# Optimization experiments

Hardware: AMD Instinct MI355X
Metric: run time of the kernel (lower is better)

## Reference

```python
import jax, jax.numpy as jnp
import numpy as np

EPS = 1e-6


def setup_inputs() -> dict:
    key = jax.random.key(0)
    ks = jax.random.split(key, 5)
    B, NH, S, DQK, DV = 2, 8, 1024, 256, 512
    return {
        "q": jax.random.normal(ks[0], (B, NH, S, DQK), dtype=jnp.float32),
        "k": jax.random.normal(ks[1], (B, NH, S, DQK), dtype=jnp.float32),
        "v": jax.random.normal(ks[2], (B, NH, S, DV), dtype=jnp.float32),
        "i_preact": jax.random.normal(ks[3], (B, NH, S), dtype=jnp.float32),
        "f_preact": jax.random.normal(ks[4], (B, NH, S), dtype=jnp.float32),
    }


def reference(q, k, v, i_preact, f_preact):
    B, NH, S, DQK = q.shape
    DV = v.shape[-1]
    inv_sqrt_d = jnp.asarray(1.0 / np.sqrt(DQK), dtype=q.dtype)
    eps = jnp.asarray(EPS, dtype=q.dtype)

    C0 = jnp.zeros((B, NH, DQK, DV), dtype=q.dtype)
    n0 = jnp.zeros((B, NH, DQK), dtype=q.dtype)
    m0 = jnp.zeros((B, NH), dtype=q.dtype)

    def step(carry, xs):
        C, n, m = carry
        q_t, k_t, v_t, i_t, f_t = xs  # [B,NH,DQK],[B,NH,DQK],[B,NH,DV],[B,NH],[B,NH]
        # f_log = -log(1 + exp(-f)) = log_sigmoid(f)
        f_log = jax.nn.log_sigmoid(f_t)
        m_new = jnp.maximum(f_log + m, i_t)
        f_gate = jnp.exp(f_log + m - m_new)
        i_gate = jnp.exp(i_t - m_new)
        kv_outer = k_t[..., :, None] * v_t[..., None, :]  # [B,NH,DQK,DV]
        C = f_gate[..., None, None] * C + i_gate[..., None, None] * kv_outer
        n = f_gate[..., None] * n + i_gate[..., None] * k_t
        q_scaled = q_t * inv_sqrt_d
        h_num = jnp.einsum("bhdv,bhd->bhv", C, q_scaled)
        qn_dot = jnp.sum(n * q_scaled, axis=-1, keepdims=True)  # [B,NH,1]
        h_den = jnp.maximum(jnp.abs(qn_dot), jnp.exp(-m_new)[..., None]) + eps
        h_t = h_num / h_den
        return (C, n, m_new), h_t

    # time-major scan over S
    xs = (
        jnp.moveaxis(q, 2, 0),
        jnp.moveaxis(k, 2, 0),
        jnp.moveaxis(v, 2, 0),
        jnp.moveaxis(i_preact, 2, 0),
        jnp.moveaxis(f_preact, 2, 0),
    )
    (C, n, m), h_tm = jax.lax.scan(step, (C0, n0, m0), xs)
    h = jnp.moveaxis(h_tm, 0, 2)  # [B,NH,S,DV]
    return h, C, n, m
```

## Files before the change

### kernel.cpp

```cpp
#include <hip/hip_runtime.h>
#include <math.h>

#define SEQ   1024
#define DQ    256
#define DVD   512
#define NHH   16
#define EPSF  1e-6f
#define INV_SQRT_D 0.0625f

typedef __attribute__((ext_vector_type(8)))  short short8v;
typedef __attribute__((ext_vector_type(16))) float f32x16;

#define WS_FG    0
#define WS_IG    (NHH*SEQ)
#define WS_ELIM  (2*NHH*SEQ)
#define WS_HDEN  (3*NHH*SEQ)
#define WS_AT    (4*NHH*SEQ)
#define WS_CS    (5*NHH*SEQ)
#define WS_AC    (6*NHH*SEQ)
#define WS_BVEC  (WS_AC + NHH*16)
#define WS_SMALL_FLOATS (WS_BVEC + NHH*16*DQ)

#define QBF_OFF  ((size_t)WS_SMALL_FLOATS * 4)
#define KBF_OFF  (QBF_OFF + (size_t)NHH*SEQ*DQ*2)
#define VTB_OFF  (KBF_OFF + (size_t)NHH*SEQ*DQ*2)
#define KUT_OFF  (VTB_OFF + (size_t)NHH*DVD*SEQ*2)

__device__ __forceinline__ unsigned short f2bf(float f) {
  unsigned int u = __float_as_uint(f);
  return (unsigned short)((u + 0x7fffu + ((u >> 16) & 1u)) >> 16);
}

__device__ __forceinline__ void gl_lds16(const void* g, void* l) {
  __builtin_amdgcn_global_load_lds(
      (const __attribute__((address_space(1))) unsigned int*)g,
      (__attribute__((address_space(3))) unsigned int*)l, 16, 0, 0);
}

__global__ __launch_bounds__(256) void prep_kernel(
    const float* __restrict__ kin, const float* __restrict__ vin,
    const float* __restrict__ ipre, const float* __restrict__ fpre,
    float* __restrict__ ws,
    unsigned short* __restrict__ k_bf, unsigned short* __restrict__ vt_bf,
    unsigned short* __restrict__ kut, float* __restrict__ m_out) {
  __shared__ float lk[64][257];
  __shared__ float swsum[4], swmax[4];
  __shared__ float bndF[16], bndM[16], fin2[2];
  __shared__ float cfg[64], cig[64], cut[64];

  const int b = blockIdx.x;
  if (b < 256) {
    const int hh = b >> 4, c = b & 15;
    const int d = threadIdx.x;
    const int lane = d & 63, wid = d >> 6;
    const int tbase = hh*SEQ + c*64;
    const size_t base = (size_t)tbase * DQ;

    #pragma unroll 4
    for (int tt = 0; tt < 64; ++tt) {
      const float val = kin[base + (size_t)tt*DQ + d];
      lk[tt][d] = val;
      k_bf[base + (size_t)tt*DQ + d] = f2bf(val);
    }

    const float4 f4 = *(const float4*)(fpre + hh*SEQ + 4*d);
    const float4 i4 = *(const float4*)(ipre + hh*SEQ + 4*d);
    float fv[4] = {f4.x, f4.y, f4.z, f4.w};
    float iv[4] = {i4.x, i4.y, i4.z, i4.w};
    float fl[4], F[4];
    float s = 0.f;
    #pragma unroll
    for (int j = 0; j < 4; ++j) {
      fl[j] = fminf(fv[j], 0.f) - log1pf(expf(-fabsf(fv[j])));
      s += fl[j]; F[j] = s;
    }
    float wsc = s;
    #pragma unroll
    for (int off = 1; off < 64; off <<= 1) {
      float o = __shfl_up(wsc, off, 64);
      if (lane >= off) wsc += o;
    }
    if (lane == 63) swsum[wid] = wsc;
    __syncthreads();
    float woff = 0.f;
    #pragma unroll
    for (int i = 0; i < 4; ++i) { float t = swsum[i]; if (i < wid) woff += t; }
    const float Fexc = woff + (wsc - s);
    #pragma unroll
    for (int j = 0; j < 4; ++j) F[j] += Fexc;

    float zser[4];
    float zs = -INFINITY;
    #pragma unroll
    for (int j = 0; j < 4; ++j) {
      zs = fmaxf(zs, iv[j] - F[j]); zser[j] = zs;
    }
    float zmI = zs;
    #pragma unroll
    for (int off = 1; off < 64; off <<= 1) {
      float o = __shfl_up(zmI, off, 64);
      if (lane >= off) zmI = fmaxf(zmI, o);
    }
    if (lane == 63) swmax[wid] = zmI;
    float zexcl = __shfl_up(zmI, 1, 64);
    if (lane == 0) zexcl = -INFINITY;
    __syncthreads();
    float zoffW = -INFINITY;
    #pragma unroll
    for (int i = 0; i < 4; ++i) { float t = swmax[i]; if (i < wid) zoffW = fmaxf(zoffW, t); }
    const float zPexc = fmaxf(zoffW, zexcl);

    float mprev = Fexc + fmaxf(zPexc, 0.f);
    float m_[4], fg_[4], ig_[4];
    #pragma unroll
    for (int j = 0; j < 4; ++j) {
      const float zP = fmaxf(zPexc, zser[j]);
      m_[j] = F[j] + fmaxf(zP, 0.f);
      fg_[j] = expf(fl[j] + mprev - m_[j]);
      ig_[j] = expf(iv[j] - m_[j]);
      mprev = m_[j];
    }

    if ((d & 15) == 15) { bndF[d >> 4] = F[3]; bndM[d >> 4] = m_[3]; }
    if (d == 255)       { fin2[0] = F[3]; fin2[1] = m_[3]; }
    const int q0 = d - 16*c;
    if (q0 >= 0 && q0 < 16) {
      #pragma unroll
      for (int j = 0; j < 4; ++j) { cfg[q0*4 + j] = fg_[j]; cig[q0*4 + j] = ig_[j]; }
    }
    if (c == 0) {
      float4 o;
      o.x=fg_[0]; o.y=fg_[1]; o.z=fg_[2]; o.w=fg_[3];
      *(float4*)(ws + WS_FG + hh*SEQ + 4*d) = o;
      o.x=ig_[0]; o.y=ig_[1]; o.z=ig_[2]; o.w=ig_[3];
      *(float4*)(ws + WS_IG + hh*SEQ + 4*d) = o;
      o.x=expf(-m_[0]); o.y=expf(-m_[1]); o.z=expf(-m_[2]); o.w=expf(-m_[3]);
      *(float4*)(ws + WS_ELIM + hh*SEQ + 4*d) = o;
      o.x=F[0]-m_[0]; o.y=F[1]-m_[1]; o.z=F[2]-m_[2]; o.w=F[3]-m_[3];
      *(float4*)(ws + WS_AT + hh*SEQ + 4*d) = o;
      o.x=iv[0]-F[0]; o.y=iv[1]-F[1]; o.z=iv[2]-F[2]; o.w=iv[3]-F[3];
      *(float4*)(ws + WS_CS + hh*SEQ + 4*d) = o;
      if (d == 255) m_out[hh] = m_[3];
    }
    __syncthreads();
    if (c == 0 && d < 16) {
      const float Fp = d ? bndF[d-1] : 0.f;
      const float mp = d ? bndM[d-1] : 0.f;
      ws[WS_AC + hh*16 + d] = expf((bndF[d] - Fp) + (mp - bndM[d]));
    }
    if (q0 >= 0 && q0 < 16) {
      const float Fe = fin2[0], me = fin2[1];
      #pragma unroll
      for (int j = 0; j < 4; ++j)
        cut[q0*4 + j] = expf(Fe - F[j] + iv[j] - me);
    }
    __syncthreads();

    float nb = 0.f;
    #pragma unroll 8
    for (int tt = 0; tt < 64; ++tt) nb = cfg[tt]*nb + cig[tt]*lk[tt][d];
    ws[WS_BVEC + (hh*16 + c)*DQ + d] = nb;
    #pragma unroll
    for (int g = 0; g < 8; ++g) {
      short8v pk;
      #pragma unroll
      for (int j = 0; j < 8; ++j) {
        const int tt = g*8 + j;
        pk[j] = (short)f2bf(cut[tt] * lk[tt][d]);
      }
      *(short8v*)(kut + ((size_t)(hh*DQ + d))*SEQ + c*64 + g*8) = pk;
    }
  } else {
    const int b2 = b - 256;
    const int hh = b2 >> 5, tg = b2 & 31;
    const int tx = threadIdx.x & 31, ty = threadIdx.x >> 5;
    float (*tile)[33] = (float(*)[33])lk;
    for (int vt = 0; vt < 16; ++vt) {
      #pragma unroll
      for (int i = 0; i < 4; ++i)
        tile[ty + 8*i][tx] =
            vin[((size_t)(hh*SEQ + tg*32 + ty + 8*i))*DVD + vt*32 + tx];
      __syncthreads();
      #pragma unroll
      for (int i = 0; i < 4; ++i)
        vt_bf[((size_t)(hh*DVD + vt*32 + ty + 8*i))*SEQ + tg*32 + tx] =
            f2bf(tile[tx][ty + 8*i]);
      __syncthreads();
    }
  }
}

__global__ __launch_bounds__(256) void hden_kernel(
    const float* __restrict__ kin, const float* __restrict__ qin,
    float* __restrict__ ws, unsigned short* __restrict__ q_bf,
    float* __restrict__ n_out) {
  const int hh = blockIdx.x >> 4;
  const int c  = blockIdx.x & 15;
  const int d  = threadIdx.x;
  __shared__ float pbuf[64][DQ];
  __shared__ float spart[64][4];

  float n = 0.f;
  for (int j = 0; j < c; ++j)
    n = ws[WS_AC + hh*16 + j]*n + ws[WS_BVEC + (hh*16 + j)*DQ + d];
  if (c == 15) {
    const float nf = ws[WS_AC + hh*16 + 15]*n +
                     ws[WS_BVEC + (hh*16 + 15)*DQ + d];
    n_out[hh*DQ + d] = nf;
  }

  const int tbase = hh*SEQ + c*64;
  const size_t base = (size_t)tbase * DQ;
  #pragma unroll 4
  for (int tt = 0; tt < 64; ++tt) {
    const float fg = ws[WS_FG + tbase + tt];
    const float ig = ws[WS_IG + tbase + tt];
    n = fg*n + ig*kin[base + (size_t)tt*DQ + d];
    const float qv = qin[base + (size_t)tt*DQ + d];
    q_bf[base + (size_t)tt*DQ + d] = f2bf(qv * INV_SQRT_D);
    pbuf[tt][d] = n * qv;
  }
  __syncthreads();

  {
    const int tt = d >> 2, qd = d & 3;
    float s = 0.f;
    #pragma unroll 8
    for (int j = 0; j < 64; ++j)
      s += pbuf[tt][qd*64 + ((j + d) & 63)];
    spart[tt][qd] = s;
  }
  __syncthreads();
  if (d < 64) {
    const float tot = (spart[d][0] + spart[d][1]) + (spart[d][2] + spart[d][3]);
    const float qn = tot * INV_SQRT_D;
    const float hd = fmaxf(fabsf(qn), ws[WS_ELIM + tbase + d]) + EPSF;
    ws[WS_HDEN + tbase + d] = hd;
  }
}

__global__ __launch_bounds__(512, 2) void attn_kernel(
    const unsigned short* __restrict__ q_bf,
    const unsigned short* __restrict__ k_bf,
    const unsigned short* __restrict__ vt_bf,
    const float* __restrict__ ws,
    float* __restrict__ h_out) {
  const int idx = blockIdx.x;
  const int hh = idx & 15;
  const int pr = (idx >> 4) & 7;
  const int vh = idx >> 7;

  const int tid = threadIdx.x;
  const int w = tid >> 6, lane = tid & 63, l31 = lane & 31, hl = lane >> 5;
  const int tsub = w >> 2;
  const int sblk = w & 3;
  const int vsub = w & 3;

  __shared__ unsigned short Klds[128*256];
  __shared__ unsigned short Vtlds[256*128];
  __shared__ unsigned short Plds[64*128];
  __shared__ float c_lds[128];

  const float* a_g  = ws + WS_AT;
  const float* c_g  = ws + WS_CS;
  const float* hd_g = ws + WS_HDEN;

  auto stage = [&](int c) {
    const int s0 = c*128;
    #pragma unroll
    for (int p = 0; p < 8; ++p) {
      int u = p*512 + tid;
      int row = u >> 5, slot = u & 31;
      const unsigned short* src = k_bf +
          ((size_t)(hh*SEQ + s0 + row))*DQ + ((slot ^ (row & 31))*8);
      gl_lds16(src, (char*)Klds + (p*8 + w)*1024);
    }
    #pragma unroll
    for (int p = 0; p < 8; ++p) {
      int u = p*512 + tid;
      int row = u >> 4, slot = u & 15;
      const unsigned short* src = vt_bf +
          ((size_t)(hh*DVD + vh*256 + row))*SEQ + s0 + ((slot ^ (row & 15))*8);
      gl_lds16(src, (char*)Vtlds + (p*8 + w)*1024);
    }
    if (tid < 128) c_lds[tid] = c_g[hh*SEQ + s0 + tid];
  };

  for (int tile = 0; tile < 2; ++tile) {
    const int qi  = tile ? pr : (15 - pr);
    const int nch = (qi >> 1) + 1;

    const int tq = qi*64 + tsub*32 + l31;
    const float a_t = a_g[hh*SEQ + tq];
    short8v qfrag[16];
    #pragma unroll
    for (int d = 0; d < 16; ++d)
      qfrag[d] = *(const short8v*)(q_bf + ((size_t)(hh*SEQ + tq))*DQ + d*16 + hl*8);

    f32x16 acc0 = {}, acc1 = {};

    stage(0);
    __syncthreads();

    for (int c = 0; c < nch; ++c) {
      const int s0 = c*128;
      f32x16 sacc = {};
      const int srow = sblk*32 + l31;
      #pragma unroll
      for (int d = 0; d < 16; ++d) {
        short8v af = *(const short8v*)&Klds[srow*256 + (((d*2 + hl) ^ (srow & 31))*8)];
        sacc = __builtin_amdgcn_mfma_f32_32x32x16_bf16(af, qfrag[d], sacc, 0, 0, 0);
      }
      const int prow = tsub*32 + l31;
      #pragma unroll
      for (int i = 0; i < 8; ++i) {
        const int r0 = 2*i;
        const int sl = sblk*32 + (r0 & 3) + 8*(r0 >> 2) + 4*hl;
        const int sg = s0 + sl;
        const float c0 = c_lds[sl];
        const float c1 = c_lds[sl + 1];
        const float p0 = (sg     <= tq) ? __expf(a_t + c0) * sacc[r0]     : 0.f;
        const float p1 = (sg + 1 <= tq) ? __expf(a_t + c1) * sacc[r0 + 1] : 0.f;
        unsigned int pk;
        asm volatile("v_cvt_pk_bf16_f32 %0, %1, %2" : "=v"(pk) : "v"(p0), "v"(p1));
        const int byte = sl*2;
        const int slot = byte >> 4, rem = byte & 15;
        *(unsigned int*)((char*)Plds + prow*256 + ((slot ^ (prow & 15))<<4) + rem) = pk;
      }
      __syncthreads();

      #pragma unroll
      for (int ss = 0; ss < 8; ++ss) {
        const int arow = tsub*32 + l31;
        short8v pa = *(const short8v*)&Plds[arow*128 + (((ss*2 + hl) ^ (arow & 15))*8)];
        const int vr0 = vsub*64 + l31;
        const int slotB = (ss*2 + hl) ^ (l31 & 15);
        short8v vb0 = *(const short8v*)&Vtlds[vr0*128 + slotB*8];
        short8v vb1 = *(const short8v*)&Vtlds[(vr0 + 32)*128 + slotB*8];
        acc0 = __builtin_amdgcn_mfma_f32_32x32x16_bf16(pa, vb0, acc0, 0, 0, 0);
        acc1 = __builtin_amdgcn_mfma_f32_32x32x16_bf16(pa, vb1, acc1, 0, 0, 0);
      }
      __syncthreads();
      if (c + 1 < nch) { stage(c + 1); __syncthreads(); }
    }

    #pragma unroll
    for (int r = 0; r < 16; ++r) {
      const int tl = tsub*32 + (r & 3) + 8*(r >> 2) + 4*hl;
      const int tg = qi*64 + tl;
      const float inv = 1.0f / hd_g[hh*SEQ + tg];
      const size_t ob = ((size_t)(hh*SEQ + tg))*DVD + vh*256 + vsub*64 + l31;
      h_out[ob]      = acc0[r] * inv;
      h_out[ob + 32] = acc1[r] * inv;
    }
  }
}

__global__ __launch_bounds__(256, 2) void cgemm_kernel(
    const unsigned short* __restrict__ kut,
    const unsigned short* __restrict__ vt,
    float* __restrict__ C_out) {
  const int b = blockIdx.x;
  const int hh = b >> 4;
  const int mt = (b >> 3) & 1;
  const int nt = b & 7;
  const int tid = threadIdx.x;
  const int w = tid >> 6, lane = tid & 63, l31 = lane & 31, hl = lane >> 5;
  const int mr = w >> 1;
  const int nc = w & 1;

  __shared__ unsigned short Alds[128*64];
  __shared__ unsigned short Blds[64*64];

  f32x16 acc0 = {}, acc1 = {};
  for (int c = 0; c < 16; ++c) {
    const int t0 = c*64;
    #pragma unroll
    for (int p = 0; p < 4; ++p) {
      int u = p*256 + tid; int row = u >> 3, slot = u & 7;
      const unsigned short* src = kut +
          ((size_t)(hh*DQ + mt*128 + row))*SEQ + t0 + ((slot ^ (row & 7))*8);
      gl_lds16(src, (char*)Alds + (p*4 + w)*1024);
    }
    #pragma unroll
    for (int p = 0; p < 2; ++p) {
      int u = p*256 + tid; int row = u >> 3, slot = u & 7;
      const unsigned short* src = vt +
          ((size_t)(hh*DVD + nt*64 + row))*SEQ + t0 + ((slot ^ (row & 7))*8);
      gl_lds16(src, (char*)Blds + (p*4 + w)*1024);
    }
    __syncthreads();
    #pragma unroll
    for (int ks = 0; ks < 4; ++ks) {
      const int br = nc*32 + l31;
      short8v bf_ = *(const short8v*)&Blds[br*64 + (((ks*2 + hl) ^ (br & 7))*8)];
      const int ar0 = mr*64 + l31, ar1 = ar0 + 32;
      short8v a0 = *(const short8v*)&Alds[ar0*64 + (((ks*2 + hl) ^ (ar0 & 7))*8)];
      short8v a1 = *(const short8v*)&Alds[ar1*64 + (((ks*2 + hl) ^ (ar1 & 7))*8)];
      acc0 = __builtin_amdgcn_mfma_f32_32x32x16_bf16(a0, bf_, acc0, 0, 0, 0);
      acc1 = __builtin_amdgcn_mfma_f32_32x32x16_bf16(a1, bf_, acc1, 0, 0, 0);
    }
    __syncthreads();
  }
  #pragma unroll
  for (int r = 0; r < 16; ++r) {
    const int dl = (r & 3) + 8*(r >> 2) + 4*hl;
    const int d0 = mt*128 + mr*64 + dl;
    const size_t ob = ((size_t)(hh*DQ + d0))*DVD + nt*64 + nc*32 + l31;
    C_out[ob]            = acc0[r];
    C_out[ob + 32*DVD]   = acc1[r];
  }
}

extern "C" void kernel_launch(void* const* d_in, const int* in_sizes, int n_in,
                              void* d_out, int out_size, void* d_ws, size_t ws_size,
                              hipStream_t stream) {
  const float* q  = (const float*)d_in[0];
  const float* k  = (const float*)d_in[1];
  const float* v  = (const float*)d_in[2];
  const float* ip = (const float*)d_in[3];
  const float* fp = (const float*)d_in[4];

  float* h_out = (float*)d_out;
  float* C_out = h_out + (size_t)NHH*SEQ*DVD;
  float* n_out = C_out + (size_t)NHH*DQ*DVD;
  float* m_out = n_out + NHH*DQ;
  float* ws    = (float*)d_ws;

  unsigned short* q_bf  = (unsigned short*)((char*)d_ws + QBF_OFF);
  unsigned short* k_bf  = (unsigned short*)((char*)d_ws + KBF_OFF);
  unsigned short* vt_bf = (unsigned short*)((char*)d_ws + VTB_OFF);
  unsigned short* kut   = (unsigned short*)((char*)d_ws + KUT_OFF);

  prep_kernel<<<768, 256, 0, stream>>>(k, v, ip, fp, ws, k_bf, vt_bf, kut, m_out);
  hden_kernel<<<NHH*16, 256, 0, stream>>>(k, q, ws, q_bf, n_out);
  attn_kernel<<<256, 512, 0, stream>>>(q_bf, k_bf, vt_bf, ws, h_out);
  cgemm_kernel<<<256, 256, 0, stream>>>(kut, vt_bf, C_out);
}
```

Baseline: 99.73 us.

## Split attention work into one query tile per block and stream V from global

```diff
diff --git a/kernel.cpp b/kernel.cpp
--- a/kernel.cpp
+++ b/kernel.cpp
@@ -239,16 +239,20 @@
   }
 }
 
-__global__ __launch_bounds__(512, 2) void attn_kernel(
+__global__ __launch_bounds__(512, 4) void attn_kernel(
     const unsigned short* __restrict__ q_bf,
     const unsigned short* __restrict__ k_bf,
     const unsigned short* __restrict__ vt_bf,
     const float* __restrict__ ws,
     float* __restrict__ h_out) {
-  const int idx = blockIdx.x;
+  const int b = blockIdx.x;
+  const int phase = b >> 8;
+  const int idx = b & 255;
   const int hh = idx & 15;
-  const int pr = (idx >> 4) & 7;
-  const int vh = idx >> 7;
+  const int vh = (idx >> 4) & 1;
+  const int qq = idx >> 5;
+  const int qi = phase ? (15 - qq) : qq;
+  const int nch = (qi >> 1) + 1;
 
   const int tid = threadIdx.x;
   const int w = tid >> 6, lane = tid & 63, l31 = lane & 31, hl = lane >> 5;
@@ -257,15 +261,23 @@
   const int vsub = w & 3;
 
   __shared__ unsigned short Klds[128*256];
-  __shared__ unsigned short Vtlds[256*128];
   __shared__ unsigned short Plds[64*128];
-  __shared__ float c_lds[128];
 
   const float* a_g  = ws + WS_AT;
-  const float* c_g  = ws + WS_CS;
+  const float* c_g  = ws + WS_CS + hh*SEQ;
   const float* hd_g = ws + WS_HDEN;
 
-  auto stage = [&](int c) {
+  const int tq = qi*64 + tsub*32 + l31;
+  const float a_t = a_g[hh*SEQ + tq];
+  const unsigned short* qp = q_bf + ((size_t)(hh*SEQ + tq))*DQ + hl*8;
+
+  const int vr0 = vsub*64 + l31;
+  const unsigned short* vp0 = vt_bf + ((size_t)(hh*DVD + vh*256 + vr0))*SEQ + hl*8;
+  const unsigned short* vp1 = vp0 + (size_t)32*SEQ;
+
+  f32x16 acc0 = {}, acc1 = {};
+
+  auto stageK = [&](int c) {
     const int s0 = c*128;
     #pragma unroll
     for (int p = 0; p < 8; ++p) {
@@ -275,84 +287,65 @@
           ((size_t)(hh*SEQ + s0 + row))*DQ + ((slot ^ (row & 31))*8);
       gl_lds16(src, (char*)Klds + (p*8 + w)*1024);
     }
-    #pragma unroll
-    for (int p = 0; p < 8; ++p) {
-      int u = p*512 + tid;
-      int row = u >> 4, slot = u & 15;
-      const unsigned short* src = vt_bf +
-          ((size_t)(hh*DVD + vh*256 + row))*SEQ + s0 + ((slot ^ (row & 15))*8);
-      gl_lds16(src, (char*)Vtlds + (p*8 + w)*1024);
-    }
-    if (tid < 128) c_lds[tid] = c_g[hh*SEQ + s0 + tid];
   };
 
-  for (int tile = 0; tile < 2; ++tile) {
-    const int qi  = tile ? pr : (15 - pr);
-    const int nch = (qi >> 1) + 1;
-
-    const int tq = qi*64 + tsub*32 + l31;
-    const float a_t = a_g[hh*SEQ + tq];
-    short8v qfrag[16];
-    #pragma unroll
-    for (int d = 0; d < 16; ++d)
-      qfrag[d] = *(const short8v*)(q_bf + ((size_t)(hh*SEQ + tq))*DQ + d*16 + hl*8);
-
-    f32x16 acc0 = {}, acc1 = {};
-
-    stage(0);
-    __syncthreads();
-
-    for (int c = 0; c < nch; ++c) {
-      const int s0 = c*128;
-      f32x16 sacc = {};
-      const int srow = sblk*32 + l31;
-      #pragma unroll
-      for (int d = 0; d < 16; ++d) {
-        short8v af = *(const short8v*)&Klds[srow*256 + (((d*2 + hl) ^ (srow & 31))*8)];
-        sacc = __builtin_amdgcn_mfma_f32_32x32x16_bf16(af, qfrag[d], sacc, 0, 0, 0);
-      }
-      const int prow = tsub*32 + l31;
-      #pragma unroll
-      for (int i = 0; i < 8; ++i) {
-        const int r0 = 2*i;
-        const int sl = sblk*32 + (r0 & 3) + 8*(r0 >> 2) + 4*hl;
-        const int sg = s0 + sl;
-        const float c0 = c_lds[sl];
-        const float c1 = c_lds[sl + 1];
-        const float p0 = (sg     <= tq) ? __expf(a_t + c0) * sacc[r0]     : 0.f;
-        const float p1 = (sg + 1 <= tq) ? __expf(a_t + c1) * sacc[r0 + 1] : 0.f;
-        unsigned int pk;
-        asm volatile("v_cvt_pk_bf16_f32 %0, %1, %2" : "=v"(pk) : "v"(p0), "v"(p1));
-        const int byte = sl*2;
-        const int slot = byte >> 4, rem = byte & 15;
-        *(unsigned int*)((char*)Plds + prow*256 + ((slot ^ (prow & 15))<<4) + rem) = pk;
-      }
-      __syncthreads();
-
-      #pragma unroll
-      for (int ss = 0; ss < 8; ++ss) {
-        const int arow = tsub*32 + l31;
-        short8v pa = *(const short8v*)&Plds[arow*128 + (((ss*2 + hl) ^ (arow & 15))*8)];
-        const int vr0 = vsub*64 + l31;
-        const int slotB = (ss*2 + hl) ^ (l31 & 15);
-        short8v vb0 = *(const short8v*)&Vtlds[vr0*128 + slotB*8];
-        short8v vb1 = *(const short8v*)&Vtlds[(vr0 + 32)*128 + slotB*8];
-        acc0 = __builtin_amdgcn_mfma_f32_32x32x16_bf16(pa, vb0, acc0, 0, 0, 0);
-        acc1 = __builtin_amdgcn_mfma_f32_32x32x16_bf16(pa, vb1, acc1, 0, 0, 0);
-      }
-      __syncthreads();
-      if (c + 1 < nch) { stage(c + 1); __syncthreads(); }
-    }
-
-    #pragma unroll
-    for (int r = 0; r < 16; ++r) {
-      const int tl = tsub*32 + (r & 3) + 8*(r >> 2) + 4*hl;
-      const int tg = qi*64 + tl;
-      const float inv = 1.0f / hd_g[hh*SEQ + tg];
-      const size_t ob = ((size_t)(hh*SEQ + tg))*DVD + vh*256 + vsub*64 + l31;
-      h_out[ob]      = acc0[r] * inv;
-      h_out[ob + 32] = acc1[r] * inv;
-    }
+  stageK(0);
+  __syncthreads();
+
+  for (int c = 0; c < nch; ++c) {
+    const int s0 = c*128;
+    f32x16 sacc = {};
+    const int srow = sblk*32 + l31;
+    #pragma unroll
+    for (int d = 0; d < 16; ++d) {
+      short8v qf = *(const short8v*)(qp + d*16);
+      short8v af = *(const short8v*)&Klds[srow*256 + (((d*2 + hl) ^ (srow & 31))*8)];
+      sacc = __builtin_amdgcn_mfma_f32_32x32x16_bf16(af, qf, sacc, 0, 0, 0);
+    }
+    const int prow = tsub*32 + l31;
+    #pragma unroll
+    for (int i = 0; i < 8; ++i) {
+      const int r0 = 2*i;
+      const int sl = sblk*32 + (r0 & 3) + 8*(r0 >> 2) + 4*hl;
+      const int sg = s0 + sl;
+      const float c0 = c_g[sg];
+      const float c1 = c_g[sg + 1];
+      const float p0 = (sg     <= tq) ? __expf(a_t + c0) * sacc[r0]     : 0.f;
+      const float p1 = (sg + 1 <= tq) ? __expf(a_t + c1) * sacc[r0 + 1] : 0.f;
+      unsigned int pk;
+      asm volatile("v_cvt_pk_bf16_f32 %0, %1, %2" : "=v"(pk) : "v"(p0), "v"(p1));
+      const int byte = sl*2;
+      const int slot = byte >> 4, rem = byte & 15;
+      *(unsigned int*)((char*)Plds + prow*256 + ((slot ^ (prow & 15))<<4) + rem) = pk;
+    }
+    __syncthreads();
+
+    short8v vf0[8], vf1[8];
+    #pragma unroll
+    for (int ss = 0; ss < 8; ++ss) {
+      vf0[ss] = *(const short8v*)(vp0 + s0 + ss*16);
+      vf1[ss] = *(const short8v*)(vp1 + s0 + ss*16);
+    }
+    if (c + 1 < nch) stageK(c + 1);
+
+    #pragma unroll
+    for (int ss = 0; ss < 8; ++ss) {
+      const int arow = tsub*32 + l31;
+      short8v pa = *(const short8v*)&Plds[arow*128 + (((ss*2 + hl) ^ (arow & 15))*8)];
+      acc0 = __builtin_amdgcn_mfma_f32_32x32x16_bf16(pa, vf0[ss], acc0, 0, 0, 0);
+      acc1 = __builtin_amdgcn_mfma_f32_32x32x16_bf16(pa, vf1[ss], acc1, 0, 0, 0);
+    }
+    __syncthreads();
+  }
+
+  #pragma unroll
+  for (int r = 0; r < 16; ++r) {
+    const int tl = tsub*32 + (r & 3) + 8*(r >> 2) + 4*hl;
+    const int tg = qi*64 + tl;
+    const float inv = 1.0f / hd_g[hh*SEQ + tg];
+    const size_t ob = ((size_t)(hh*SEQ + tg))*DVD + vh*256 + vsub*64 + l31;
+    h_out[ob]      = acc0[r] * inv;
+    h_out[ob + 32] = acc1[r] * inv;
   }
 }
 
@@ -434,6 +427,6 @@
 
   prep_kernel<<<768, 256, 0, stream>>>(k, v, ip, fp, ws, k_bf, vt_bf, kut, m_out);
   hden_kernel<<<NHH*16, 256, 0, stream>>>(k, q, ws, q_bf, n_out);
-  attn_kernel<<<256, 512, 0, stream>>>(q_bf, k_bf, vt_bf, ws, h_out);
+  attn_kernel<<<512, 512, 0, stream>>>(q_bf, k_bf, vt_bf, ws, h_out);
   cgemm_kernel<<<256, 256, 0, stream>>>(kut, vt_bf, C_out);
 }
```

Measured after the change: 208.4 us. 109% more time.

## Merge hden and C-gemm into one launch and split attention tiles per block

Applied to the files above, without the earlier changes.

```diff
diff --git a/kernel.cpp b/kernel.cpp
--- a/kernel.cpp
+++ b/kernel.cpp
@@ -190,52 +190,110 @@
   }
 }
 
-__global__ __launch_bounds__(256) void hden_kernel(
+__global__ __launch_bounds__(256) void aux_kernel(
     const float* __restrict__ kin, const float* __restrict__ qin,
     float* __restrict__ ws, unsigned short* __restrict__ q_bf,
-    float* __restrict__ n_out) {
-  const int hh = blockIdx.x >> 4;
-  const int c  = blockIdx.x & 15;
-  const int d  = threadIdx.x;
-  __shared__ float pbuf[64][DQ];
-  __shared__ float spart[64][4];
-
-  float n = 0.f;
-  for (int j = 0; j < c; ++j)
-    n = ws[WS_AC + hh*16 + j]*n + ws[WS_BVEC + (hh*16 + j)*DQ + d];
-  if (c == 15) {
-    const float nf = ws[WS_AC + hh*16 + 15]*n +
-                     ws[WS_BVEC + (hh*16 + 15)*DQ + d];
-    n_out[hh*DQ + d] = nf;
-  }
-
-  const int tbase = hh*SEQ + c*64;
-  const size_t base = (size_t)tbase * DQ;
-  #pragma unroll 4
-  for (int tt = 0; tt < 64; ++tt) {
-    const float fg = ws[WS_FG + tbase + tt];
-    const float ig = ws[WS_IG + tbase + tt];
-    n = fg*n + ig*kin[base + (size_t)tt*DQ + d];
-    const float qv = qin[base + (size_t)tt*DQ + d];
-    q_bf[base + (size_t)tt*DQ + d] = f2bf(qv * INV_SQRT_D);
-    pbuf[tt][d] = n * qv;
-  }
-  __syncthreads();
-
-  {
-    const int tt = d >> 2, qd = d & 3;
-    float s = 0.f;
-    #pragma unroll 8
-    for (int j = 0; j < 64; ++j)
-      s += pbuf[tt][qd*64 + ((j + d) & 63)];
-    spart[tt][qd] = s;
-  }
-  __syncthreads();
-  if (d < 64) {
-    const float tot = (spart[d][0] + spart[d][1]) + (spart[d][2] + spart[d][3]);
-    const float qn = tot * INV_SQRT_D;
-    const float hd = fmaxf(fabsf(qn), ws[WS_ELIM + tbase + d]) + EPSF;
-    ws[WS_HDEN + tbase + d] = hd;
+    float* __restrict__ n_out,
+    const unsigned short* __restrict__ kut,
+    const unsigned short* __restrict__ vt,
+    float* __restrict__ C_out) {
+  __shared__ __align__(16) char smem[66560];
+  const int b = blockIdx.x;
+
+  if (b < 256) {
+    float (*pbuf)[DQ] = (float(*)[DQ])smem;
+    float (*spart)[4] = (float(*)[4])(smem + 65536);
+    const int hh = b >> 4;
+    const int c  = b & 15;
+    const int d  = threadIdx.x;
+
+    float n = 0.f;
+    for (int j = 0; j < c; ++j)
+      n = ws[WS_AC + hh*16 + j]*n + ws[WS_BVEC + (hh*16 + j)*DQ + d];
+    if (c == 15) {
+      const float nf = ws[WS_AC + hh*16 + 15]*n +
+                       ws[WS_BVEC + (hh*16 + 15)*DQ + d];
+      n_out[hh*DQ + d] = nf;
+    }
+
+    const int tbase = hh*SEQ + c*64;
+    const size_t base = (size_t)tbase * DQ;
+    #pragma unroll 4
+    for (int tt = 0; tt < 64; ++tt) {
+      const float fg = ws[WS_FG + tbase + tt];
+      const float ig = ws[WS_IG + tbase + tt];
+      n = fg*n + ig*kin[base + (size_t)tt*DQ + d];
+      const float qv = qin[base + (size_t)tt*DQ + d];
+      q_bf[base + (size_t)tt*DQ + d] = f2bf(qv * INV_SQRT_D);
+      pbuf[tt][d] = n * qv;
+    }
+    __syncthreads();
+
+    {
+      const int tt = d >> 2, qd = d & 3;
+      float s = 0.f;
+      #pragma unroll 8
+      for (int j = 0; j < 64; ++j)
+        s += pbuf[tt][qd*64 + ((j + d) & 63)];
+      spart[tt][qd] = s;
+    }
+    __syncthreads();
+    if (d < 64) {
+      const float tot = (spart[d][0] + spart[d][1]) + (spart[d][2] + spart[d][3]);
+      const float qn = tot * INV_SQRT_D;
+      const float hd = fmaxf(fabsf(qn), ws[WS_ELIM + tbase + d]) + EPSF;
+      ws[WS_HDEN + tbase + d] = hd;
+    }
+  } else {
+    unsigned short* Alds = (unsigned short*)smem;
+    unsigned short* Blds = (unsigned short*)(smem + 16384);
+    const int b2 = b - 256;
+    const int hh = b2 >> 4;
+    const int mt = (b2 >> 3) & 1;
+    const int nt = b2 & 7;
+    const int tid = threadIdx.x;
+    const int w = tid >> 6, lane = tid & 63, l31 = lane & 31, hl = lane >> 5;
+    const int mr = w >> 1;
+    const int nc = w & 1;
+
+    f32x16 acc0 = {}, acc1 = {};
+    for (int c = 0; c < 16; ++c) {
+      const int t0 = c*64;
+      #pragma unroll
+      for (int p = 0; p < 4; ++p) {
+        int u = p*256 + tid; int row = u >> 3, slot = u & 7;
+        const unsigned short* src = kut +
+            ((size_t)(hh*DQ + mt*128 + row))*SEQ + t0 + ((slot ^ (row & 7))*8);
+        gl_lds16(src, (char*)Alds + (p*4 + w)*1024);
+      }
+      #pragma unroll
+      for (int p = 0; p < 2; ++p) {
+        int u = p*256 + tid; int row = u >> 3, slot = u & 7;
+        const unsigned short* src = vt +
+            ((size_t)(hh*DVD + nt*64 + row))*SEQ + t0 + ((slot ^ (row & 7))*8);
+        gl_lds16(src, (char*)Blds + (p*4 + w)*1024);
+      }
+      __syncthreads();
+      #pragma unroll
+      for (int ks = 0; ks < 4; ++ks) {
+        const int br = nc*32 + l31;
+        short8v bf_ = *(const short8v*)&Blds[br*64 + (((ks*2 + hl) ^ (br & 7))*8)];
+        const int ar0 = mr*64 + l31, ar1 = ar0 + 32;
+        short8v a0 = *(const short8v*)&Alds[ar0*64 + (((ks*2 + hl) ^ (ar0 & 7))*8)];
+        short8v a1 = *(const short8v*)&Alds[ar1*64 + (((ks*2 + hl) ^ (ar1 & 7))*8)];
+        acc0 = __builtin_amdgcn_mfma_f32_32x32x16_bf16(a0, bf_, acc0, 0, 0, 0);
+        acc1 = __builtin_amdgcn_mfma_f32_32x32x16_bf16(a1, bf_, acc1, 0, 0, 0);
+      }
+      __syncthreads();
+    }
+    #pragma unroll
+    for (int r = 0; r < 16; ++r) {
+      const int dl = (r & 3) + 8*(r >> 2) + 4*hl;
+      const int d0 = mt*128 + mr*64 + dl;
+      const size_t ob = ((size_t)(hh*DQ + d0))*DVD + nt*64 + nc*32 + l31;
+      C_out[ob]            = acc0[r];
+      C_out[ob + 32*DVD]   = acc1[r];
+    }
   }
 }
 
@@ -245,10 +303,14 @@
     const unsigned short* __restrict__ vt_bf,
     const float* __restrict__ ws,
     float* __restrict__ h_out) {
-  const int idx = blockIdx.x;
+  const int b = blockIdx.x;
+  const int phase = b >> 8;
+  const int idx = b & 255;
   const int hh = idx & 15;
-  const int pr = (idx >> 4) & 7;
-  const int vh = idx >> 7;
+  const int vh = (idx >> 4) & 1;
+  const int qq = idx >> 5;
+  const int qi = phase ? (15 - qq) : qq;
+  const int nch = (qi >> 1) + 1;
 
   const int tid = threadIdx.x;
   const int w = tid >> 6, lane = tid & 63, l31 = lane & 31, hl = lane >> 5;
@@ -264,6 +326,16 @@
   const float* a_g  = ws + WS_AT;
   const float* c_g  = ws + WS_CS;
   const float* hd_g = ws + WS_HDEN;
+
+  const int tq = qi*64 + tsub*32 + l31;
+  const float a_t = a_g[hh*SEQ + tq];
+
+  short8v qfrag[16];
+  #pragma unroll
+  for (int d = 0; d < 16; ++d)
+    qfrag[d] = *(const short8v*)(q_bf + ((size_t)(hh*SEQ + tq))*DQ + d*16 + hl*8);
+
+  f32x16 acc0 = {}, acc1 = {};
 
   auto stage = [&](int c) {
     const int s0 = c*128;
@@ -286,129 +358,59 @@
     if (tid < 128) c_lds[tid] = c_g[hh*SEQ + s0 + tid];
   };
 
-  for (int tile = 0; tile < 2; ++tile) {
-    const int qi  = tile ? pr : (15 - pr);
-    const int nch = (qi >> 1) + 1;
-
-    const int tq = qi*64 + tsub*32 + l31;
-    const float a_t = a_g[hh*SEQ + tq];
-    short8v qfrag[16];
-    #pragma unroll
-    for (int d = 0; d < 16; ++d)
-      qfrag[d] = *(const short8v*)(q_bf + ((size_t)(hh*SEQ + tq))*DQ + d*16 + hl*8);
-
-    f32x16 acc0 = {}, acc1 = {};
-
-    stage(0);
-    __syncthreads();
-
-    for (int c = 0; c < nch; ++c) {
-      const int s0 = c*128;
-      f32x16 sacc = {};
-      const int srow = sblk*32 + l31;
-      #pragma unroll
-      for (int d = 0; d < 16; ++d) {
-        short8v af = *(const short8v*)&Klds[srow*256 + (((d*2 + hl) ^ (srow & 31))*8)];
-        sacc = __builtin_amdgcn_mfma_f32_32x32x16_bf16(af, qfrag[d], sacc, 0, 0, 0);
-      }
-      const int prow = tsub*32 + l31;
-      #pragma unroll
-      for (int i = 0; i < 8; ++i) {
-        const int r0 = 2*i;
-        const int sl = sblk*32 + (r0 & 3) + 8*(r0 >> 2) + 4*hl;
-        const int sg = s0 + sl;
-        const float c0 = c_lds[sl];
-        const float c1 = c_lds[sl + 1];
-        const float p0 = (sg     <= tq) ? __expf(a_t + c0) * sacc[r0]     : 0.f;
-        const float p1 = (sg + 1 <= tq) ? __expf(a_t + c1) * sacc[r0 + 1] : 0.f;
-        unsigned int pk;
-        asm volatile("v_cvt_pk_bf16_f32 %0, %1, %2" : "=v"(pk) : "v"(p0), "v"(p1));
-        const int byte = sl*2;
-        const int slot = byte >> 4, rem = byte & 15;
-        *(unsigned int*)((char*)Plds + prow*256 + ((slot ^ (prow & 15))<<4) + rem) = pk;
-      }
-      __syncthreads();
-
-      #pragma unroll
-      for (int ss = 0; ss < 8; ++ss) {
-        const int arow = tsub*32 + l31;
-        short8v pa = *(const short8v*)&Plds[arow*128 + (((ss*2 + hl) ^ (arow & 15))*8)];
-        const int vr0 = vsub*64 + l31;
-        const int slotB = (ss*2 + hl) ^ (l31 & 15);
-        short8v vb0 = *(const short8v*)&Vtlds[vr0*128 + slotB*8];
-        short8v vb1 = *(const short8v*)&Vtlds[(vr0 + 32)*128 + slotB*8];
-        acc0 = __builtin_amdgcn_mfma_f32_32x32x16_bf16(pa, vb0, acc0, 0, 0, 0);
-        acc1 = __builtin_amdgcn_mfma_f32_32x32x16_bf16(pa, vb1, acc1, 0, 0, 0);
-      }
-      __syncthreads();
-      if (c + 1 < nch) { stage(c + 1); __syncthreads(); }
-    }
-
-    #pragma unroll
-    for (int r = 0; r < 16; ++r) {
-      const int tl = tsub*32 + (r & 3) + 8*(r >> 2) + 4*hl;
-      const int tg = qi*64 + tl;
-      const float inv = 1.0f / hd_g[hh*SEQ + tg];
-      const size_t ob = ((size_t)(hh*SEQ + tg))*DVD + vh*256 + vsub*64 + l31;
-      h_out[ob]      = acc0[r] * inv;
-      h_out[ob + 32] = acc1[r] * inv;
-    }
+  stage(0);
+  __syncthreads();
+
+  for (int c = 0; c < nch; ++c) {
+    const int s0 = c*128;
+    f32x16 sacc = {};
+    const int srow = sblk*32 + l31;
+    #pragma unroll
+    for (int d = 0; d < 16; ++d) {
+      short8v af = *(const short8v*)&Klds[srow*256 + (((d*2 + hl) ^ (srow & 31))*8)];
+      sacc = __builtin_amdgcn_mfma_f32_32x32x16_bf16(af, qfrag[d], sacc, 0, 0, 0);
+    }
+    const int prow = tsub*32 + l31;
+    #pragma unroll
+    for (int i = 0; i < 8; ++i) {
+      const int r0 = 2*i;
+      const int sl = sblk*32 + (r0 & 3) + 8*(r0 >> 2) + 4*hl;
+      const int sg = s0 + sl;
+      const float c0 = c_lds[sl];
+      const float c1 = c_lds[sl + 1];
+      const float p0 = (sg     <= tq) ? __expf(a_t + c0) * sacc[r0]     : 0.f;
+      const float p1 = (sg + 1 <= tq) ? __expf(a_t + c1) * sacc[r0 + 1] : 0.f;
+      unsigned int pk;
+      asm volatile("v_cvt_pk_bf16_f32 %0, %1, %2" : "=v"(pk) : "v"(p0), "v"(p1));
+      const int byte = sl*2;
+      const int slot = byte >> 4, rem = byte & 15;
+      *(unsigned int*)((char*)Plds + prow*256 + ((slot ^ (prow & 15))<<4) + rem) = pk;
+    }
+    __syncthreads();
+
+    #pragma unroll
+    for (int ss = 0; ss < 8; ++ss) {
+      const int arow = tsub*32 + l31;
+      short8v pa = *(const short8v*)&Plds[arow*128 + (((ss*2 + hl) ^ (arow & 15))*8)];
+      const int vr0 = vsub*64 + l31;
+      const int slotB = (ss*2 + hl) ^ (l31 & 15);
+      short8v vb0 = *(const short8v*)&Vtlds[vr0*128 + slotB*8];
+      short8v vb1 = *(const short8v*)&Vtlds[(vr0 + 32)*128 + slotB*8];
+      acc0 = __builtin_amdgcn_mfma_f32_32x32x16_bf16(pa, vb0, acc0, 0, 0, 0);
+      acc1 = __builtin_amdgcn_mfma_f32_32x32x16_bf16(pa, vb1, acc1, 0, 0, 0);
+    }
+    __syncthreads();
+    if (c + 1 < nch) { stage(c + 1); __syncthreads(); }
   }
-}
-
-__global__ __launch_bounds__(256, 2) void cgemm_kernel(
-    const unsigned short* __restrict__ kut,
-    const unsigned short* __restrict__ vt,
-    float* __restrict__ C_out) {
-  const int b = blockIdx.x;
-  const int hh = b >> 4;
-  const int mt = (b >> 3) & 1;
-  const int nt = b & 7;
-  const int tid = threadIdx.x;
-  const int w = tid >> 6, lane = tid & 63, l31 = lane & 31, hl = lane >> 5;
-  const int mr = w >> 1;
-  const int nc = w & 1;
-
-  __shared__ unsigned short Alds[128*64];
-  __shared__ unsigned short Blds[64*64];
-
-  f32x16 acc0 = {}, acc1 = {};
-  for (int c = 0; c < 16; ++c) {
-    const int t0 = c*64;
-    #pragma unroll
-    for (int p = 0; p < 4; ++p) {
-      int u = p*256 + tid; int row = u >> 3, slot = u & 7;
-      const unsigned short* src = kut +
-          ((size_t)(hh*DQ + mt*128 + row))*SEQ + t0 + ((slot ^ (row & 7))*8);
-      gl_lds16(src, (char*)Alds + (p*4 + w)*1024);
-    }
-    #pragma unroll
-    for (int p = 0; p < 2; ++p) {
-      int u = p*256 + tid; int row = u >> 3, slot = u & 7;
-      const unsigned short* src = vt +
-          ((size_t)(hh*DVD + nt*64 + row))*SEQ + t0 + ((slot ^ (row & 7))*8);
-      gl_lds16(src, (char*)Blds + (p*4 + w)*1024);
-    }
-    __syncthreads();
-    #pragma unroll
-    for (int ks = 0; ks < 4; ++ks) {
-      const int br = nc*32 + l31;
-      short8v bf_ = *(const short8v*)&Blds[br*64 + (((ks*2 + hl) ^ (br & 7))*8)];
-      const int ar0 = mr*64 + l31, ar1 = ar0 + 32;
-      short8v a0 = *(const short8v*)&Alds[ar0*64 + (((ks*2 + hl) ^ (ar0 & 7))*8)];
-      short8v a1 = *(const short8v*)&Alds[ar1*64 + (((ks*2 + hl) ^ (ar1 & 7))*8)];
-      acc0 = __builtin_amdgcn_mfma_f32_32x32x16_bf16(a0, bf_, acc0, 0, 0, 0);
-      acc1 = __builtin_amdgcn_mfma_f32_32x32x16_bf16(a1, bf_, acc1, 0, 0, 0);
-    }
-    __syncthreads();
-  }
+
   #pragma unroll
   for (int r = 0; r < 16; ++r) {
-    const int dl = (r & 3) + 8*(r >> 2) + 4*hl;
-    const int d0 = mt*128 + mr*64 + dl;
-    const size_t ob = ((size_t)(hh*DQ + d0))*DVD + nt*64 + nc*32 + l31;
-    C_out[ob]            = acc0[r];
-    C_out[ob + 32*DVD]   = acc1[r];
+    const int tl = tsub*32 + (r & 3) + 8*(r >> 2) + 4*hl;
+    const int tg = qi*64 + tl;
+    const float inv = 1.0f / hd_g[hh*SEQ + tg];
+    const size_t ob = ((size_t)(hh*SEQ + tg))*DVD + vh*256 + vsub*64 + l31;
+    h_out[ob]      = acc0[r] * inv;
+    h_out[ob + 32] = acc1[r] * inv;
   }
 }
 
@@ -433,7 +435,6 @@
   unsigned short* kut   = (unsigned short*)((char*)d_ws + KUT_OFF);
 
   prep_kernel<<<768, 256, 0, stream>>>(k, v, ip, fp, ws, k_bf, vt_bf, kut, m_out);
-  hden_kernel<<<NHH*16, 256, 0, stream>>>(k, q, ws, q_bf, n_out);
-  attn_kernel<<<256, 512, 0, stream>>>(q_bf, k_bf, vt_bf, ws, h_out);
-  cgemm_kernel<<<256, 256, 0, stream>>>(kut, vt_bf, C_out);
-}
+  aux_kernel<<<512, 256, 0, stream>>>(k, q, ws, q_bf, n_out, kut, vt_bf, C_out);
+  attn_kernel<<<512, 512, 0, stream>>>(q_bf, k_bf, vt_bf, ws, h_out);
+}
```

After: 88.89 us. -10.9%, faster.
